# Kernel tuning notes

Measured on AMD Instinct MI355X. Metric: run time of the kernel, lower is better.

The kernel has to match this reference:

```python
import jax, jax.numpy as jnp
import numpy as np

H, W = 256, 832
B = 2
SEARCH_W, SEARCH_H = 7, 3
SPARSITY_RAD = 2
SENSE_RANGE = 10
PIX_W = 20.0          # pixel_distance_weight
ALPHA_W = 0.7         # alpha_distance_weight
MULLINE_W = 15.0      # pixel_mulline_distance_weight
ALPHA_PAD = 0.6       # alpha_padding
INF = 1e9


def _sorted_offsets(span_x, span_y):
    xs, ys = np.meshgrid(span_x, span_y)
    xs = xs.flatten(); ys = ys.flatten()
    order = np.argsort(xs ** 2 + ys ** 2, kind='stable')
    return xs[order].astype(np.int32), ys[order].astype(np.int32)


def setup_inputs() -> dict:
    key = jax.random.key(0)
    k1, k2 = jax.random.split(key)
    src = (jax.random.uniform(k1, (B, 1, H, W)) < 0.02).astype(jnp.float32)
    dst = (jax.random.uniform(k2, (B, 1, H, W)) < 0.02).astype(jnp.float32)
    xx, yy = _sorted_offsets(np.arange(-SEARCH_W, SEARCH_W + 1), np.arange(-SEARCH_H, SEARCH_H + 1))
    sxs, sys_ = np.meshgrid(np.arange(-SPARSITY_RAD, SPARSITY_RAD + 1), np.arange(-SPARSITY_RAD, SPARSITY_RAD + 1))
    sxx = sxs.flatten().astype(np.int32); syy = sys_.flatten().astype(np.int32)
    cxx, cyy = _sorted_offsets(np.arange(-SENSE_RANGE, SENSE_RANGE + 1), np.arange(-SENSE_RANGE, SENSE_RANGE + 1))
    return {"binMapsrc": src, "binMapdst": dst,
            "xx": jnp.asarray(xx), "yy": jnp.asarray(yy),
            "sxx": jnp.asarray(sxx), "syy": jnp.asarray(syy),
            "cxx": jnp.asarray(cxx), "cyy": jnp.asarray(cyy)}


def _orientation(m):
    # local edge orientation from a 3x3 box-blurred map
    b = sum(jnp.roll(jnp.roll(m, di, 0), dj, 1) for di in (-1, 0, 1) for dj in (-1, 0, 1))
    gy, gx = jnp.gradient(b)
    return jnp.arctan2(gy, gx)


def _morph_single(src, dst, xx, yy, sxx, syy, cxx, cyy):
    gy, gx = jnp.meshgrid(jnp.arange(H, dtype=jnp.int32), jnp.arange(W, dtype=jnp.int32), indexing='ij')

    def gather(offy, offx, arr, fill):
        ii = gy[None] + offy[:, None, None]          # [K,H,W]
        jj = gx[None] + offx[:, None, None]
        inb = (ii >= 0) & (ii < H) & (jj >= 0) & (jj < W)
        vals = arr[jnp.clip(ii, 0, H - 1), jnp.clip(jj, 0, W - 1)]
        return jnp.where(inb, vals, fill)

    src_e = src > 0.5
    # --- sparsify source edge points: keep min-linear-index edge in each sparsity window ---
    lin = jnp.where(src_e, (gy * W + gx).astype(jnp.float32), INF)
    keep = src_e & (lin == gather(syy, sxx, lin, INF).min(0))
    # --- windowed correspondence search with distance + orientation scoring ---
    theta_s = _orientation(src)
    theta_d = _orientation(dst)
    hit = gather(yy, xx, dst, 0.0) > 0.5             # [K,H,W]
    ang = 1.0 - jnp.cos(theta_s[None] - gather(yy, xx, theta_d, 0.0))
    dist = jnp.sqrt((xx * xx + yy * yy).astype(jnp.float32))
    score = jnp.where(hit, PIX_W * dist[:, None, None] + MULLINE_W * ALPHA_W * ang, INF)
    kbest = jnp.argmin(score, axis=0)                # [H,W]
    active = keep & (score.min(0) < 0.5 * INF)
    dispx = jnp.where(active, xx[kbest].astype(jnp.float32), 0.0)
    dispy = jnp.where(active, yy[kbest].astype(jnp.float32), 0.0)
    # --- diffuse sparse displacements over the sense window (scan keeps memory small) ---
    R = SENSE_RANGE
    pad = lambda a: jnp.pad(a, ((R, R), (R, R)))
    pdx, pdy, pm = pad(dispx), pad(dispy), pad(active.astype(jnp.float32))
    wk = jnp.exp(-jnp.sqrt((cxx * cxx + cyy * cyy).astype(jnp.float32)) / (0.5 * R))

    def body(carry, inp):
        nx, ny, den = carry
        dy_, dx_, w = inp
        sl = lambda a: jax.lax.dynamic_slice(a, (R + dy_, R + dx_), (H, W))
        return (nx + w * sl(pdx), ny + w * sl(pdy), den + w * sl(pm)), None

    zeros = jnp.zeros((H, W), jnp.float32)
    (nx, ny, den), _ = jax.lax.scan(body, (zeros, zeros, zeros), (cyy, cxx, wk))
    mdx = ALPHA_PAD * nx / (den + 1e-6)
    mdy = ALPHA_PAD * ny / (den + 1e-6)
    morphedx = gx.astype(jnp.float32) + mdx
    morphedy = gy.astype(jnp.float32) + mdy
    return jnp.stack([morphedx, morphedy], 0)        # [2,H,W]


def reference(binMapsrc, binMapdst, xx, yy, sxx, syy, cxx, cyy):
    f = lambda s, d: _morph_single(s, d, xx, yy, sxx, syy, cxx, cyy)
    return jax.vmap(f)(binMapsrc[:, 0], binMapdst[:, 0])  # [B,2,H,W]
```

## Files before the change

### kernel.cpp

```cpp
#include <hip/hip_runtime.h>
#include <math.h>

#define BB 2
#define HH 256
#define WW 832
#define HWIMG (HH * WW)

#define TS 32
#define TXN (WW / TS)
#define TYN (HH / TS)
#define RG 52
#define RGPX (RG * RG)
#define KCAP 256

__device__ inline float theta_at(const float* __restrict__ m, int i, int j) {
    int ri[5], cj[5];
#pragma unroll
    for (int t = 0; t < 5; ++t) {
        int r = i + t - 2; r = (r < 0) ? r + HH : (r >= HH ? r - HH : r);
        int c = j + t - 2; c = (c < 0) ? c + WW : (c >= WW ? c - WW : c);
        ri[t] = r * WW; cj[t] = c;
    }
    float S[5][5];
#pragma unroll
    for (int a = 0; a < 5; ++a)
#pragma unroll
        for (int c = 0; c < 5; ++c)
            S[a][c] = m[ri[a] + cj[c]];
    float ct[5], cm[5], cb[5];
#pragma unroll
    for (int c = 0; c < 5; ++c) {
        ct[c] = S[0][c] + S[1][c] + S[2][c];
        cm[c] = S[1][c] + S[2][c] + S[3][c];
        cb[c] = S[2][c] + S[3][c] + S[4][c];
    }
    float Bm = ct[1] + ct[2] + ct[3];
    float Bp = cb[1] + cb[2] + cb[3];
    float Bl = cm[0] + cm[1] + cm[2];
    float Br = cm[2] + cm[3] + cm[4];
    float Bc = cm[1] + cm[2] + cm[3];
    float gy = (i == 0) ? (Bp - Bc) : (i == HH - 1) ? (Bc - Bm) : 0.5f * (Bp - Bm);
    float gx = (j == 0) ? (Br - Bc) : (j == WW - 1) ? (Bc - Bl) : 0.5f * (Br - Bl);
    return atan2f(gy, gx);
}

__global__ __launch_bounds__(1024) void fused_kernel(
        const float* __restrict__ src, const float* __restrict__ dst,
        const int* __restrict__ xx, const int* __restrict__ yy, int K,
        float* __restrict__ out) {
    __shared__ int kox[128], koy[128];
    __shared__ float kd[128];
    __shared__ int recs[KCAP];
    __shared__ float tss[KCAP];
    __shared__ float4 ent[KCAP];
    __shared__ float wt[441];
    __shared__ int nkeep, ne;

    int tid = threadIdx.x;
    if (tid == 0) { nkeep = 0; ne = 0; }
    for (int t = tid; t < K; t += 1024) {
        int ox = xx[t], oy = yy[t];
        kox[t] = ox; koy[t] = oy;
        kd[t] = 20.0f * sqrtf((float)(ox * ox + oy * oy));
    }
    for (int t = tid; t < 441; t += 1024) {
        int dy = t / 21 - 10;
        int dx = t % 21 - 10;
        wt[t] = expf(-sqrtf((float)(dx * dx + dy * dy)) / 5.0f);
    }

    int b = blockIdx.z;
    int i0 = blockIdx.y * TS;
    int j0 = blockIdx.x * TS;
    const float* sb = src + b * HWIMG;
    const float* db = dst + b * HWIMG;
    __syncthreads();

    for (int t = tid; t < RGPX; t += 1024) {
        int gi = i0 - 10 + t / RG;
        int gj = j0 - 10 + t % RG;
        if (gi < 0 || gi >= HH || gj < 0 || gj >= WW) continue;
        if (sb[gi * WW + gj] > 0.5f) {
            float m = 0.f;
#pragma unroll
            for (int p = 0; p < 12; ++p) {
                int di = (p < 5) ? -2 : (p < 10 ? -1 : 0);
                int dj = (p < 5) ? (p - 2) : (p < 10 ? (p - 7) : (p - 12));
                int ii = gi + di, jj = gj + dj;
                bool inb = (ii >= 0) && (jj >= 0) && (jj < WW);
                float v = sb[inb ? (ii * WW + jj) : 0];
                m = fmaxf(m, inb ? v : 0.f);
            }
            if (m <= 0.5f) {
                float ts = theta_at(sb, gi, gj);
                int pos = atomicAdd(&nkeep, 1);
                if (pos < KCAP) { recs[pos] = gj | (gi << 10); tss[pos] = ts; }
            }
        }
    }
    __syncthreads();

    int nk = (nkeep < KCAP) ? nkeep : KCAP;
    int lane = tid & 63;
    int wv = tid >> 6;
    for (int w = wv; w < nk; w += 16) {
        int rec = recs[w];
        int kj = rec & 1023;
        int ki = rec >> 10;
        float ts = tss[w];

        float best = 1e9f;
        int bk = 1 << 20;
#pragma unroll
        for (int rr = 0; rr < 2; ++rr) {
            int k = lane + rr * 64;
            if (k < K) {
                int pi = ki + koy[k], pj = kj + kox[k];
                if (pi >= 0 && pi < HH && pj >= 0 && pj < WW && db[pi * WW + pj] > 0.5f) {
                    float td = theta_at(db, pi, pj);
                    float sc = kd[k] + 10.5f * (1.0f - cosf(ts - td));
                    if (sc < best || (sc == best && k < bk)) { best = sc; bk = k; }
                }
            }
        }
#pragma unroll
        for (int off = 32; off >= 1; off >>= 1) {
            float ob = __shfl_down(best, off, 64);
            int ok = __shfl_down(bk, off, 64);
            if (ob < best || (ob == best && ok < bk)) { best = ob; bk = ok; }
        }
        if (lane == 0 && best < 5e8f) {
            int pos = atomicAdd(&ne, 1);
            if (pos < KCAP)
                ent[pos] = make_float4((float)kj, (float)ki,
                                       (float)kox[bk], (float)koy[bk]);
        }
    }
    __syncthreads();

    int nn = (ne < KCAP) ? ne : KCAP;
    int gj = j0 + (tid & 31);
    int gi = i0 + (tid >> 5);
    float nx = 0.f, ny = 0.f, de = 0.f;
    for (int c = 0; c < nn; ++c) {
        float4 E = ent[c];
        int dj = (int)E.x - gj;
        int di = (int)E.y - gi;
        if (dj >= -10 && dj <= 10 && di >= -10 && di <= 10) {
            float w = wt[(di + 10) * 21 + dj + 10];
            de += w; nx += w * E.z; ny += w * E.w;
        }
    }
    float inv = 0.6f / (de + 1e-6f);
    int obase = b * 2 * HWIMG;
    out[obase + gi * WW + gj] = (float)gj + nx * inv;
    out[obase + HWIMG + gi * WW + gj] = (float)gi + ny * inv;
}

extern "C" void kernel_launch(void* const* d_in, const int* in_sizes, int n_in,
                              void* d_out, int out_size, void* d_ws, size_t ws_size,
                              hipStream_t stream) {
    const float* src = (const float*)d_in[0];
    const float* dst = (const float*)d_in[1];
    const int* xx = (const int*)d_in[2];
    const int* yy = (const int*)d_in[3];
    int K = in_sizes[2];

    float* out = (float*)d_out;
    dim3 grid(TXN, TYN, BB);
    fused_kernel<<<grid, dim3(1024), 0, stream>>>(src, dst, xx, yy, K, out);
}
```

Before: 108.6 us.

## Stage src and dst halo tiles in LDS for sparsify and matching

Loads padded src (56x56) and dst (62x72) halo regions into shared memory with float4 loads. The sparsity check, orientation stencils and destination edge lookups then read LDS instead of scattered global memory, falling back to the global theta path only near image borders. This targets repeated uncoalesced global reads in the 5x5 stencils, at the cost of extra LDS footprint and an up-front staging pass.

```diff
diff --git a/kernel.cpp b/kernel.cpp
--- a/kernel.cpp
+++ b/kernel.cpp
@@ -9,9 +9,12 @@
 #define TS 32
 #define TXN (WW / TS)
 #define TYN (HH / TS)
-#define RG 52
-#define RGPX (RG * RG)
 #define KCAP 256
+
+#define SRH 56
+#define SRW 56
+#define DRH 62
+#define DRW 72
 
 __device__ inline float theta_at(const float* __restrict__ m, int i, int j) {
     int ri[5], cj[5];
@@ -44,10 +47,53 @@
     return atan2f(gy, gx);
 }
 
+__device__ inline float theta_lds(const float* __restrict__ m, int stride,
+                                  int li, int lj) {
+    const float* p = m + (li - 2) * stride + (lj - 2);
+    float S[5][5];
+#pragma unroll
+    for (int a = 0; a < 5; ++a)
+#pragma unroll
+        for (int c = 0; c < 5; ++c)
+            S[a][c] = p[a * stride + c];
+    float ct[5], cm[5], cb[5];
+#pragma unroll
+    for (int c = 0; c < 5; ++c) {
+        ct[c] = S[0][c] + S[1][c] + S[2][c];
+        cm[c] = S[1][c] + S[2][c] + S[3][c];
+        cb[c] = S[2][c] + S[3][c] + S[4][c];
+    }
+    float Bm = ct[1] + ct[2] + ct[3];
+    float Bp = cb[1] + cb[2] + cb[3];
+    float Bl = cm[0] + cm[1] + cm[2];
+    float Br = cm[2] + cm[3] + cm[4];
+    float gy = 0.5f * (Bp - Bm);
+    float gx = 0.5f * (Br - Bl);
+    return atan2f(gy, gx);
+}
+
+__device__ inline float4 load4_guard(const float* __restrict__ img, int r, int c0) {
+    float4 v = make_float4(0.f, 0.f, 0.f, 0.f);
+    if (r >= 0 && r < HH) {
+        if (c0 >= 0 && c0 + 3 < WW) {
+            v = *(const float4*)(img + r * WW + c0);
+        } else {
+            const float* rp = img + r * WW;
+            if (c0 + 0 >= 0 && c0 + 0 < WW) v.x = rp[c0 + 0];
+            if (c0 + 1 >= 0 && c0 + 1 < WW) v.y = rp[c0 + 1];
+            if (c0 + 2 >= 0 && c0 + 2 < WW) v.z = rp[c0 + 2];
+            if (c0 + 3 >= 0 && c0 + 3 < WW) v.w = rp[c0 + 3];
+        }
+    }
+    return v;
+}
+
 __global__ __launch_bounds__(1024) void fused_kernel(
         const float* __restrict__ src, const float* __restrict__ dst,
         const int* __restrict__ xx, const int* __restrict__ yy, int K,
         float* __restrict__ out) {
+    __shared__ float4 slds4[SRH * SRW / 4];
+    __shared__ float4 dlds4[DRH * DRW / 4];
     __shared__ int kox[128], koy[128];
     __shared__ float kd[128];
     __shared__ int recs[KCAP];
@@ -55,44 +101,54 @@
     __shared__ float4 ent[KCAP];
     __shared__ float wt[441];
     __shared__ int nkeep, ne;
+    float* slds = (float*)slds4;
+    float* dlds = (float*)dlds4;
 
     int tid = threadIdx.x;
-    if (tid == 0) { nkeep = 0; ne = 0; }
-    for (int t = tid; t < K; t += 1024) {
-        int ox = xx[t], oy = yy[t];
-        kox[t] = ox; koy[t] = oy;
-        kd[t] = 20.0f * sqrtf((float)(ox * ox + oy * oy));
-    }
-    for (int t = tid; t < 441; t += 1024) {
-        int dy = t / 21 - 10;
-        int dx = t % 21 - 10;
-        wt[t] = expf(-sqrtf((float)(dx * dx + dy * dy)) / 5.0f);
-    }
-
     int b = blockIdx.z;
     int i0 = blockIdx.y * TS;
     int j0 = blockIdx.x * TS;
     const float* sb = src + b * HWIMG;
     const float* db = dst + b * HWIMG;
+
+    if (tid == 0) { nkeep = 0; ne = 0; }
+
+#pragma unroll
+    for (int t = tid; t < SRH * (SRW / 4); t += 1024)
+        slds4[t] = load4_guard(sb, (i0 - 12) + t / (SRW / 4),
+                               (j0 - 12) + (t % (SRW / 4)) * 4);
+    for (int t = tid; t < DRH * (DRW / 4); t += 1024)
+        dlds4[t] = load4_guard(db, (i0 - 15) + t / (DRW / 4),
+                               (j0 - 20) + (t % (DRW / 4)) * 4);
+
+    for (int t = tid; t < K; t += 1024) {
+        int ox = xx[t], oy = yy[t];
+        kox[t] = ox; koy[t] = oy;
+        kd[t] = 20.0f * sqrtf((float)(ox * ox + oy * oy));
+    }
+    for (int t = tid; t < 441; t += 1024) {
+        int dy = t / 21 - 10;
+        int dx = t % 21 - 10;
+        wt[t] = expf(-sqrtf((float)(dx * dx + dy * dy)) / 5.0f);
+    }
     __syncthreads();
 
-    for (int t = tid; t < RGPX; t += 1024) {
-        int gi = i0 - 10 + t / RG;
-        int gj = j0 - 10 + t % RG;
-        if (gi < 0 || gi >= HH || gj < 0 || gj >= WW) continue;
-        if (sb[gi * WW + gj] > 0.5f) {
+    for (int t = tid; t < 52 * 52; t += 1024) {
+        int rl = t / 52, cl = t % 52;
+        int li = rl + 2, lj = cl + 2;
+        if (slds[li * SRW + lj] > 0.5f) {
             float m = 0.f;
 #pragma unroll
             for (int p = 0; p < 12; ++p) {
                 int di = (p < 5) ? -2 : (p < 10 ? -1 : 0);
                 int dj = (p < 5) ? (p - 2) : (p < 10 ? (p - 7) : (p - 12));
-                int ii = gi + di, jj = gj + dj;
-                bool inb = (ii >= 0) && (jj >= 0) && (jj < WW);
-                float v = sb[inb ? (ii * WW + jj) : 0];
-                m = fmaxf(m, inb ? v : 0.f);
+                m = fmaxf(m, slds[(li + di) * SRW + (lj + dj)]);
             }
             if (m <= 0.5f) {
-                float ts = theta_at(sb, gi, gj);
+                int gi = i0 - 10 + rl, gj = j0 - 10 + cl;
+                bool inner = (gi >= 2) && (gi < HH - 2) && (gj >= 2) && (gj < WW - 2);
+                float ts = inner ? theta_lds(slds, SRW, li, lj)
+                                 : theta_at(sb, gi, gj);
                 int pos = atomicAdd(&nkeep, 1);
                 if (pos < KCAP) { recs[pos] = gj | (gi << 10); tss[pos] = ts; }
             }
@@ -108,6 +164,8 @@
         int kj = rec & 1023;
         int ki = rec >> 10;
         float ts = tss[w];
+        int kli = ki - i0 + 15;
+        int klj = kj - j0 + 20;
 
         float best = 1e9f;
         int bk = 1 << 20;
@@ -115,9 +173,12 @@
         for (int rr = 0; rr < 2; ++rr) {
             int k = lane + rr * 64;
             if (k < K) {
-                int pi = ki + koy[k], pj = kj + kox[k];
-                if (pi >= 0 && pi < HH && pj >= 0 && pj < WW && db[pi * WW + pj] > 0.5f) {
-                    float td = theta_at(db, pi, pj);
+                int pli = kli + koy[k], plj = klj + kox[k];
+                if (dlds[pli * DRW + plj] > 0.5f) {
+                    int pi = ki + koy[k], pj = kj + kox[k];
+                    bool inner = (pi >= 2) && (pi < HH - 2) && (pj >= 2) && (pj < WW - 2);
+                    float td = inner ? theta_lds(dlds, DRW, pli, plj)
+                                     : theta_at(db, pi, pj);
                     float sc = kd[k] + 10.5f * (1.0f - cosf(ts - td));
                     if (sc < best || (sc == best && k < bk)) { best = sc; bk = k; }
                 }
```

New measurement: 99.16 us. 8.7% less time.
